# Kernel tuning notes

Measured on AMD Instinct MI355X. Metric: run time of the kernel, lower is better.

The kernel has to match this reference:

```python
import jax, jax.numpy as jnp
import numpy as np
from jax import lax

B, T, L = 32, 64, 1500        # flows, max packets per flow, packet length (MTU)
H, DC = 128, 100              # lstm hidden, cnn feature dim
KS, ST = 5, 3                 # conv kernel/stride
FLAT = 54 * 32                # conv output length 1500->499->165->54, 32 channels


def setup_inputs() -> dict:
    key = jax.random.key(0)
    ks = jax.random.split(key, 12)
    s = 0.05
    X = jax.random.normal(ks[0], (B, T, L), jnp.float32)
    lengths = jax.random.randint(ks[1], (B,), 1, T + 1, dtype=jnp.int32)
    conv1_w = jax.random.normal(ks[2], (128, 1, KS), jnp.float32) * s
    conv2_w = jax.random.normal(ks[3], (32, 128, KS), jnp.float32) * s
    conv3_w = jax.random.normal(ks[4], (32, 32, KS), jnp.float32) * s
    lin_w = jax.random.normal(ks[5], (DC, FLAT), jnp.float32) * s
    w_ih0 = jax.random.normal(ks[6], (4 * H, DC), jnp.float32) * s
    w_hh0 = jax.random.normal(ks[7], (4 * H, H), jnp.float32) * s
    w_ih1 = jax.random.normal(ks[8], (4 * H, H), jnp.float32) * s
    w_hh1 = jax.random.normal(ks[9], (4 * H, H), jnp.float32) * s
    fc1_w = jax.random.normal(ks[10], (10, H), jnp.float32) * s
    fc2_w = jax.random.normal(ks[11], (2, 10), jnp.float32) * s
    return {"X": X, "lengths": lengths, "conv1_w": conv1_w, "conv2_w": conv2_w,
            "conv3_w": conv3_w, "lin_w": lin_w, "w_ih0": w_ih0, "w_hh0": w_hh0,
            "w_ih1": w_ih1, "w_hh1": w_hh1, "fc1_w": fc1_w, "fc2_w": fc2_w}


def _conv(x, w):
    # x: [N, Cin, L], w: [Cout, Cin, K] -> valid conv, stride 3 (torch Conv1d semantics)
    return lax.conv_general_dilated(x, w, (ST,), 'VALID',
                                    dimension_numbers=('NCH', 'OIH', 'NCH'))


def _lstm_layer(xs, mask, w_ih, w_hh):
    # xs: [T, B, D]; mask: [T, B] (True = valid step); no biases (bias=False)
    Bn = xs.shape[1]
    h0 = jnp.zeros((Bn, H), xs.dtype)
    c0 = jnp.zeros((Bn, H), xs.dtype)

    def step(carry, inp):
        h, c = carry
        x_t, m_t = inp
        gates = x_t @ w_ih.T + h @ w_hh.T          # [B, 4H]
        i, f, g, o = jnp.split(gates, 4, axis=-1)  # torch gate order i,f,g,o
        i, f, o = jax.nn.sigmoid(i), jax.nn.sigmoid(f), jax.nn.sigmoid(o)
        g = jnp.tanh(g)
        c_new = f * c + i * g
        h_new = o * jnp.tanh(c_new)
        m = m_t[:, None]
        h = jnp.where(m, h_new, h)  # freeze state past each flow's length
        c = jnp.where(m, c_new, c)
        return (h, c), h

    (h_f, c_f), hs = lax.scan(step, (h0, c0), (xs, mask))
    return hs, h_f


def reference(X, lengths, conv1_w, conv2_w, conv3_w, lin_w,
              w_ih0, w_hh0, w_ih1, w_hh1, fc1_w, fc2_w):
    leaky = jax.nn.leaky_relu  # slope 0.01 matches torch default
    # ODCNN over every packet (batched over all B*T packets instead of python loops)
    x = X.reshape(B * T, 1, L)
    x = leaky(_conv(x, conv1_w))   # [BT, 128, 499]
    x = leaky(_conv(x, conv2_w))   # [BT, 32, 165]
    x = leaky(_conv(x, conv3_w))   # [BT, 32, 54]
    feats = x.reshape(B * T, FLAT) @ lin_w.T          # [BT, 100] (no activation)
    feats = feats.reshape(B, T, DC).transpose(1, 0, 2)  # [T, B, 100]
    mask = jnp.arange(T)[:, None] < lengths[None, :]     # [T, B]
    hs1, _ = _lstm_layer(feats, mask, w_ih0, w_hh0)
    _, h2 = _lstm_layer(hs1, mask, w_ih1, w_hh1)         # h at step len-1, top layer
    out = leaky(h2 @ fc1_w.T)
    out = leaky(out @ fc2_w.T)                           # [B, out_dim]
    return out
```

## Files before the change

### kernel.cpp

```cpp
#include <hip/hip_runtime.h>
#include <hip/hip_bf16.h>

#define B_ 32
#define T_ 64
#define H_ 128
#define L3OUT 54
#define FLAT_ 1728

typedef __attribute__((ext_vector_type(8))) short bf16x8;
typedef __attribute__((ext_vector_type(4))) float f32x4;

__device__ __forceinline__ float leakyf(float v) { return v > 0.f ? v : 0.01f * v; }
__device__ __forceinline__ float sigmoidf_(float v) { return 1.f / (1.f + expf(-v)); }
__device__ __forceinline__ unsigned int bf16rne(float v) {
  unsigned int b = __float_as_uint(v);
  return (b + 0x7FFFu + ((b >> 16) & 1u)) >> 16;
}
__device__ __forceinline__ unsigned int pk2bf(float lo, float hi) {
  __hip_bfloat162 h2 = __float22bfloat162_rn(make_float2(lo, hi));
  return *reinterpret_cast<unsigned int*>(&h2);
}
__device__ __forceinline__ bf16x8 ldb8(const unsigned short* p) {
  return *(const bf16x8*)p;
}
__device__ __forceinline__ void barrier_lgkm() {
  asm volatile("s_waitcnt lgkmcnt(0)\n\ts_barrier" ::: "memory");
}

__global__ __launch_bounds__(256) void k_prep(
    const float* __restrict__ w1, const float* __restrict__ w2,
    const float* __restrict__ w3, const float* __restrict__ linw,
    const float* __restrict__ wih0, const float* __restrict__ whh0,
    const float* __restrict__ wih1, const float* __restrict__ whh1,
    unsigned short* __restrict__ w1eh, unsigned short* __restrict__ w1el,
    unsigned short* __restrict__ w2h, unsigned short* __restrict__ w2l,
    unsigned short* __restrict__ w3h, unsigned short* __restrict__ w3l,
    unsigned short* __restrict__ linwh, unsigned short* __restrict__ linwl,
    unsigned short* __restrict__ wih0h, unsigned short* __restrict__ wih0l,
    float* __restrict__ whh0T, float* __restrict__ wih1T,
    float* __restrict__ whh1T) {
  const int e = blockIdx.x * 256 + threadIdx.x;
  if (e >= 264960) {
    int e5 = e - 264960;
    int m = e5 >> 16, r = e5 & 65535;
    int k = r >> 9, j = r & 511;
    const float* src = (m == 0) ? whh0 : ((m == 1) ? wih1 : whh1);
    float* dst = (m == 0) ? whh0T : ((m == 1) ? wih1T : whh1T);
    dst[r] = src[j * 128 + k];
    return;
  }
  float v;
  unsigned short* dh;
  unsigned short* dl;
  int di;
  if (e < 20480) {
    int cc = e / 5120, rem = e - cc * 5120;
    int c2 = rem / 160, r = rem - c2 * 160;
    int tap = r >> 5, c1l = r & 31;
    v = w2[c2 * 640 + (cc * 32 + c1l) * 5 + tap];
    dh = w2h; dl = w2l; di = e;
  } else if (e < 25600) {
    int e2 = e - 20480;
    int c3 = e2 / 160, r = e2 - c3 * 160;
    int tap = r >> 5, c2 = r & 31;
    v = w3[c3 * 160 + c2 * 5 + tap];
    dh = w3h; dl = w3l; di = e2;
  } else if (e < 198400) {
    int e3 = e - 25600;
    v = linw[e3];
    dh = linwh; dl = linwl; di = e3;
  } else if (e < 263936) {
    int e4 = e - 198400;
    int g = e4 >> 7, k = e4 & 127;
    v = (k < 100) ? wih0[g * 100 + k] : 0.f;
    dh = wih0h; dl = wih0l; di = e4;
  } else {
    int i = e - 263936;
    int c1 = i >> 3, j = i & 7;
    v = (j < 5) ? w1[c1 * 5 + j] : 0.f;
    dh = w1eh; dl = w1el; di = i;
  }
  unsigned int hb = bf16rne(v);
  float hf = __uint_as_float(hb << 16);
  unsigned int lb = bf16rne(v - hf);
  dh[di] = (unsigned short)hb;
  dl[di] = (unsigned short)lb;
}

__global__ __launch_bounds__(512) void k_conv123(
    const float* __restrict__ X, const float* __restrict__ w1,
    const unsigned short* __restrict__ w2h, const unsigned short* __restrict__ w2l,
    const unsigned short* __restrict__ w3h, const unsigned short* __restrict__ w3l,
    unsigned short* __restrict__ s3g) {
  __shared__ __align__(16) float Xs[1504];
  __shared__ __align__(16) unsigned int AhU[10640];

  const int n = blockIdx.x;
  const int tid = threadIdx.x;
  const int lane = tid & 63;
  const int w = tid >> 6;
  const int l15 = lane & 15;
  const int cg = lane >> 4;

  const float* Xn = X + (size_t)n * 1500;
  for (int i = tid; i < 1500; i += 512) Xs[i] = Xn[i];
  if (tid < 4) Xs[1500 + tid] = 0.f;
  for (int i = tid; i < 640; i += 512) AhU[10000 + i] = 0u;
  barrier_lgkm();

  float x0 = 0.f, x1 = 0.f, x2 = 0.f, x3 = 0.f, x4 = 0.f;
  if (tid < 500) {
    const float* xp = Xs + 3 * tid;
    x0 = xp[0]; x1 = xp[1]; x2 = xp[2]; x3 = xp[3]; x4 = xp[4];
  }

  f32x4 acc2[2][2];
#pragma unroll
  for (int a = 0; a < 2; ++a)
#pragma unroll
    for (int m = 0; m < 2; ++m) acc2[a][m] = (f32x4){0.f, 0.f, 0.f, 0.f};

  for (int cc = 0; cc < 4; ++cc) {
    barrier_lgkm();
    if (tid < 500) {
      const float* wc = w1 + cc * 160;
      unsigned int rowbuf[16];
#pragma unroll
      for (int p = 0; p < 16; ++p) {
        const float* wa = wc + 10 * p;
        float vA = fmaf(x4, wa[4], fmaf(x3, wa[3], fmaf(x2, wa[2], fmaf(x1, wa[1], x0 * wa[0]))));
        float vB = fmaf(x4, wa[9], fmaf(x3, wa[8], fmaf(x2, wa[7], fmaf(x1, wa[6], x0 * wa[5]))));
        vA = fmaxf(vA, 0.01f * vA);
        vB = fmaxf(vB, 0.01f * vB);
        rowbuf[p] = pk2bf(vA, vB);
      }
#pragma unroll
      for (int q = 0; q < 4; ++q)
        *(uint4*)(&AhU[tid * 20 + 4 * q]) = *(uint4*)(&rowbuf[4 * q]);
    }
    barrier_lgkm();
    const unsigned short* w2hB = w2h + cc * 5120;
    const unsigned short* w2lB = w2l + cc * 5120;
#pragma unroll
    for (int tap = 0; tap < 5; ++tap) {
      const int wc = tap * 32 + cg * 8;
      bf16x8 ah0 = ldb8(w2hB + l15 * 160 + wc);
      bf16x8 ah1 = ldb8(w2hB + (l15 + 16) * 160 + wc);
      bf16x8 al0 = ldb8(w2lB + l15 * 160 + wc);
      bf16x8 al1 = ldb8(w2lB + (l15 + 16) * 160 + wc);
      {
        bf16x8 bfr = ldb8((const unsigned short*)AhU + (3 * (w * 16 + l15) + tap) * 40 + cg * 8);
        acc2[0][0] = __builtin_amdgcn_mfma_f32_16x16x32_bf16(ah0, bfr, acc2[0][0], 0, 0, 0);
        acc2[0][0] = __builtin_amdgcn_mfma_f32_16x16x32_bf16(al0, bfr, acc2[0][0], 0, 0, 0);
        acc2[0][1] = __builtin_amdgcn_mfma_f32_16x16x32_bf16(ah1, bfr, acc2[0][1], 0, 0, 0);
        acc2[0][1] = __builtin_amdgcn_mfma_f32_16x16x32_bf16(al1, bfr, acc2[0][1], 0, 0, 0);
      }
      if (w < 3) {
        int nt = 8 + w;
        bf16x8 bfr = ldb8((const unsigned short*)AhU + (3 * (nt * 16 + l15) + tap) * 40 + cg * 8);
        acc2[1][0] = __builtin_amdgcn_mfma_f32_16x16x32_bf16(ah0, bfr, acc2[1][0], 0, 0, 0);
        acc2[1][0] = __builtin_amdgcn_mfma_f32_16x16x32_bf16(al0, bfr, acc2[1][0], 0, 0, 0);
        acc2[1][1] = __builtin_amdgcn_mfma_f32_16x16x32_bf16(ah1, bfr, acc2[1][1], 0, 0, 0);
        acc2[1][1] = __builtin_amdgcn_mfma_f32_16x16x32_bf16(al1, bfr, acc2[1][1], 0, 0, 0);
      }
    }
  }
  barrier_lgkm();
  for (int i = tid; i < 400; i += 512) AhU[176 * 20 + i] = 0u;
#pragma unroll
  for (int nti = 0; nti < 2; ++nti) {
    int nt = (nti == 0) ? w : (8 + w);
    if (nti == 0 || w < 3) {
      int l2 = nt * 16 + l15;
#pragma unroll
      for (int mt = 0; mt < 2; ++mt) {
#pragma unroll
        for (int j = 0; j < 2; ++j) {
          float e0 = leakyf(acc2[nti][mt][2 * j]);
          float e1 = leakyf(acc2[nti][mt][2 * j + 1]);
          AhU[l2 * 20 + mt * 8 + cg * 2 + j] = pk2bf(e0, e1);
        }
      }
    }
  }
  barrier_lgkm();
  if (w < 4) {
    f32x4 a3[2];
    a3[0] = (f32x4){0.f, 0.f, 0.f, 0.f};
    a3[1] = (f32x4){0.f, 0.f, 0.f, 0.f};
#pragma unroll
    for (int tap = 0; tap < 5; ++tap) {
      const int wc = tap * 32 + cg * 8;
      bf16x8 wh0 = ldb8(w3h + l15 * 160 + wc);
      bf16x8 wh1 = ldb8(w3h + (l15 + 16) * 160 + wc);
      bf16x8 wl0 = ldb8(w3l + l15 * 160 + wc);
      bf16x8 wl1 = ldb8(w3l + (l15 + 16) * 160 + wc);
      bf16x8 bfr = ldb8((const unsigned short*)AhU + (3 * (w * 16 + l15) + tap) * 40 + cg * 8);
      a3[0] = __builtin_amdgcn_mfma_f32_16x16x32_bf16(wh0, bfr, a3[0], 0, 0, 0);
      a3[0] = __builtin_amdgcn_mfma_f32_16x16x32_bf16(wl0, bfr, a3[0], 0, 0, 0);
      a3[1] = __builtin_amdgcn_mfma_f32_16x16x32_bf16(wh1, bfr, a3[1], 0, 0, 0);
      a3[1] = __builtin_amdgcn_mfma_f32_16x16x32_bf16(wl1, bfr, a3[1], 0, 0, 0);
    }
    int l3 = w * 16 + l15;
    if (l3 < L3OUT) {
#pragma unroll
      for (int mt = 0; mt < 2; ++mt) {
#pragma unroll
        for (int r = 0; r < 4; ++r) {
          int c3 = mt * 16 + cg * 4 + r;
          s3g[(size_t)n * FLAT_ + c3 * L3OUT + l3] = (unsigned short)bf16rne(leakyf(a3[mt][r]));
        }
      }
    }
  }
}

__global__ __launch_bounds__(448) void k_gemm_fx(
    const unsigned short* __restrict__ s3g,
    const unsigned short* __restrict__ linwh, const unsigned short* __restrict__ linwl,
    const unsigned short* __restrict__ wih0h, const unsigned short* __restrict__ wih0l,
    float* __restrict__ xg0) {
  __shared__ __align__(16) unsigned short fehS[16][136];
  __shared__ __align__(16) unsigned short felS[16][136];

  const int m0 = blockIdx.x * 16;
  const int tid = threadIdx.x;
  const int lane = tid & 63;
  const int w = tid >> 6;
  const int l15 = lane & 15;
  const int cg = lane >> 4;

  if (tid < 192) {
    int r = tid / 12, c = tid - r * 12;
    ((unsigned int*)&fehS[r][112])[c] = 0u;
    ((unsigned int*)&felS[r][112])[c] = 0u;
  }

  int brow = w * 16 + l15;
  if (brow > 99) brow = 99;
  const unsigned short* ap = s3g + (size_t)(m0 + l15) * FLAT_ + cg * 8;
  const unsigned short* bhp = linwh + (size_t)brow * FLAT_ + cg * 8;
  const unsigned short* blp = linwl + (size_t)brow * FLAT_ + cg * 8;

  f32x4 acc = (f32x4){0.f, 0.f, 0.f, 0.f};
#pragma unroll 6
  for (int ks = 0; ks < 54; ++ks) {
    bf16x8 af = ldb8(ap + ks * 32);
    bf16x8 bh = ldb8(bhp + ks * 32);
    bf16x8 bl = ldb8(blp + ks * 32);
    acc = __builtin_amdgcn_mfma_f32_16x16x32_bf16(af, bh, acc, 0, 0, 0);
    acc = __builtin_amdgcn_mfma_f32_16x16x32_bf16(af, bl, acc, 0, 0, 0);
  }
  const int jcol = w * 16 + l15;
#pragma unroll
  for (int r = 0; r < 4; ++r) {
    float v = acc[r];
    unsigned int hb = bf16rne(v);
    float hf = __uint_as_float(hb << 16);
    unsigned int lb = bf16rne(v - hf);
    fehS[cg * 4 + r][jcol] = (unsigned short)hb;
    felS[cg * 4 + r][jcol] = (unsigned short)lb;
  }
  __syncthreads();

#pragma unroll
  for (int nt0 = 0; nt0 < 5; ++nt0) {
    int nt = w + 7 * nt0;
    if (nt < 32) {
      f32x4 a = (f32x4){0.f, 0.f, 0.f, 0.f};
#pragma unroll
      for (int ks = 0; ks < 4; ++ks) {
        bf16x8 ah = ldb8(&fehS[l15][ks * 32 + cg * 8]);
        bf16x8 al = ldb8(&felS[l15][ks * 32 + cg * 8]);
        int br = nt * 16 + l15;
        bf16x8 bh = ldb8(wih0h + (size_t)br * 128 + ks * 32 + cg * 8);
        bf16x8 bl = ldb8(wih0l + (size_t)br * 128 + ks * 32 + cg * 8);
        a = __builtin_amdgcn_mfma_f32_16x16x32_bf16(ah, bh, a, 0, 0, 0);
        a = __builtin_amdgcn_mfma_f32_16x16x32_bf16(ah, bl, a, 0, 0, 0);
        a = __builtin_amdgcn_mfma_f32_16x16x32_bf16(al, bh, a, 0, 0, 0);
      }
#pragma unroll
      for (int r = 0; r < 4; ++r)
        xg0[(size_t)(m0 + cg * 4 + r) * 512 + nt * 16 + l15] = a[r];
    }
  }
}

__global__ __launch_bounds__(512) void k_lstm0(
    const float* __restrict__ xg0, const float* __restrict__ whh0T,
    const int* __restrict__ lengths, float* __restrict__ hs1) {
  __shared__ __align__(16) float h0s[H_];
  __shared__ float ps[16 * 128];
  __shared__ float gs[512];
  const int b = blockIdx.x;
  const int tid = threadIdx.x;
  const int ks = tid >> 7;
  const int jj = tid & 127;
  float w[4][32];
#pragma unroll
  for (int kk = 0; kk < 32; ++kk) {
#pragma unroll
    for (int q = 0; q < 4; ++q)
      w[q][kk] = whh0T[(ks * 32 + kk) * 512 + q * 128 + jj];
  }
  if (tid < H_) h0s[tid] = 0.f;
  float c = 0.f;
  const int len = lengths[b];
  float xcur = xg0[(size_t)(b * T_) * 512 + tid];
  barrier_lgkm();
  for (int t = 0; t < len; ++t) {
    float xnxt = (t + 1 < len) ? xg0[(size_t)(b * T_ + t + 1) * 512 + tid] : 0.f;
    float p0 = 0.f, p1 = 0.f, p2 = 0.f, p3 = 0.f;
#pragma unroll
    for (int k4 = 0; k4 < 8; ++k4) {
      float4 hv = *(const float4*)(h0s + ks * 32 + k4 * 4);
      p0 = fmaf(hv.x, w[0][k4 * 4], fmaf(hv.y, w[0][k4 * 4 + 1], fmaf(hv.z, w[0][k4 * 4 + 2], fmaf(hv.w, w[0][k4 * 4 + 3], p0))));
      p1 = fmaf(hv.x, w[1][k4 * 4], fmaf(hv.y, w[1][k4 * 4 + 1], fmaf(hv.z, w[1][k4 * 4 + 2], fmaf(hv.w, w[1][k4 * 4 + 3], p1))));
      p2 = fmaf(hv.x, w[2][k4 * 4], fmaf(hv.y, w[2][k4 * 4 + 1], fmaf(hv.z, w[2][k4 * 4 + 2], fmaf(hv.w, w[2][k4 * 4 + 3], p2))));
      p3 = fmaf(hv.x, w[3][k4 * 4], fmaf(hv.y, w[3][k4 * 4 + 1], fmaf(hv.z, w[3][k4 * 4 + 2], fmaf(hv.w, w[3][k4 * 4 + 3], p3))));
    }
    ps[(ks * 4 + 0) * 128 + jj] = p0;
    ps[(ks * 4 + 1) * 128 + jj] = p1;
    ps[(ks * 4 + 2) * 128 + jj] = p2;
    ps[(ks * 4 + 3) * 128 + jj] = p3;
    barrier_lgkm();
    {
      float gsum = xcur + ((ps[(0 * 4 + ks) * 128 + jj] + ps[(1 * 4 + ks) * 128 + jj]) +
                           (ps[(2 * 4 + ks) * 128 + jj] + ps[(3 * 4 + ks) * 128 + jj]));
      gs[tid] = (ks == 2) ? tanhf(gsum) : sigmoidf_(gsum);
    }
    barrier_lgkm();
    if (tid < H_) {
      float ig = gs[jj];
      float fg = gs[128 + jj];
      float gt = gs[256 + jj];
      float og = gs[384 + jj];
      c = fg * c + ig * gt;
      float hn = og * tanhf(c);
      h0s[jj] = hn;
      hs1[((size_t)(b * T_ + t)) * H_ + jj] = hn;
    }
    barrier_lgkm();
    xcur = xnxt;
  }
}

__global__ __launch_bounds__(512) void k_xg1(
    const float* __restrict__ hs1, const float* __restrict__ wih1T,
    float* __restrict__ xg1) {
  __shared__ __align__(16) float hsS[8][128];
  const int r0 = blockIdx.x * 8;
  const int tid = threadIdx.x;
  for (int i = tid; i < 8 * 128; i += 512) ((float*)hsS)[i] = hs1[(size_t)r0 * 128 + i];
  __syncthreads();
  float acc[8] = {0.f, 0.f, 0.f, 0.f, 0.f, 0.f, 0.f, 0.f};
#pragma unroll 4
  for (int k4 = 0; k4 < 32; ++k4) {
    float w0 = wih1T[(4 * k4 + 0) * 512 + tid];
    float w1v = wih1T[(4 * k4 + 1) * 512 + tid];
    float w2v = wih1T[(4 * k4 + 2) * 512 + tid];
    float w3v = wih1T[(4 * k4 + 3) * 512 + tid];
#pragma unroll
    for (int i = 0; i < 8; ++i) {
      float4 h = *(const float4*)(&hsS[i][4 * k4]);
      acc[i] += h.x * w0 + h.y * w1v + h.z * w2v + h.w * w3v;
    }
  }
#pragma unroll
  for (int i = 0; i < 8; ++i) xg1[((size_t)(r0 + i)) * 512 + tid] = acc[i];
}

__global__ __launch_bounds__(512) void k_lstm1(
    const float* __restrict__ xg1, const float* __restrict__ whh1T,
    const float* __restrict__ fc1, const float* __restrict__ fc2,
    const int* __restrict__ lengths, float* __restrict__ out) {
  __shared__ __align__(16) float h1s[H_];
  __shared__ float ps[16 * 128];
  __shared__ float gs[512];
  __shared__ float tmp10[10];
  const int b = blockIdx.x;
  const int tid = threadIdx.x;
  const int ks = tid >> 7;
  const int jj = tid & 127;
  float w[4][32];
#pragma unroll
  for (int kk = 0; kk < 32; ++kk) {
#pragma unroll
    for (int q = 0; q < 4; ++q)
      w[q][kk] = whh1T[(ks * 32 + kk) * 512 + q * 128 + jj];
  }
  if (tid < H_) h1s[tid] = 0.f;
  float c = 0.f;
  const int len = lengths[b];
  float xcur = xg1[(size_t)(b * T_) * 512 + tid];
  barrier_lgkm();
  for (int t = 0; t < len; ++t) {
    float xnxt = (t + 1 < len) ? xg1[(size_t)(b * T_ + t + 1) * 512 + tid] : 0.f;
    float p0 = 0.f, p1 = 0.f, p2 = 0.f, p3 = 0.f;
#pragma unroll
    for (int k4 = 0; k4 < 8; ++k4) {
      float4 hv = *(const float4*)(h1s + ks * 32 + k4 * 4);
      p0 = fmaf(hv.x, w[0][k4 * 4], fmaf(hv.y, w[0][k4 * 4 + 1], fmaf(hv.z, w[0][k4 * 4 + 2], fmaf(hv.w, w[0][k4 * 4 + 3], p0))));
      p1 = fmaf(hv.x, w[1][k4 * 4], fmaf(hv.y, w[1][k4 * 4 + 1], fmaf(hv.z, w[1][k4 * 4 + 2], fmaf(hv.w, w[1][k4 * 4 + 3], p1))));
      p2 = fmaf(hv.x, w[2][k4 * 4], fmaf(hv.y, w[2][k4 * 4 + 1], fmaf(hv.z, w[2][k4 * 4 + 2], fmaf(hv.w, w[2][k4 * 4 + 3], p2))));
      p3 = fmaf(hv.x, w[3][k4 * 4], fmaf(hv.y, w[3][k4 * 4 + 1], fmaf(hv.z, w[3][k4 * 4 + 2], fmaf(hv.w, w[3][k4 * 4 + 3], p3))));
    }
    ps[(ks * 4 + 0) * 128 + jj] = p0;
    ps[(ks * 4 + 1) * 128 + jj] = p1;
    ps[(ks * 4 + 2) * 128 + jj] = p2;
    ps[(ks * 4 + 3) * 128 + jj] = p3;
    barrier_lgkm();
    {
      float gsum = xcur + ((ps[(0 * 4 + ks) * 128 + jj] + ps[(1 * 4 + ks) * 128 + jj]) +
                           (ps[(2 * 4 + ks) * 128 + jj] + ps[(3 * 4 + ks) * 128 + jj]));
      gs[tid] = (ks == 2) ? tanhf(gsum) : sigmoidf_(gsum);
    }
    barrier_lgkm();
    if (tid < H_) {
      float ig = gs[jj];
      float fg = gs[128 + jj];
      float gt = gs[256 + jj];
      float og = gs[384 + jj];
      c = fg * c + ig * gt;
      float hn = og * tanhf(c);
      h1s[jj] = hn;
    }
    barrier_lgkm();
    xcur = xnxt;
  }
  if (tid < 10) {
    const float* fr = fc1 + tid * H_;
    float s = 0.f;
#pragma unroll 4
    for (int k = 0; k < H_; ++k) s += h1s[k] * fr[k];
    tmp10[tid] = leakyf(s);
  }
  barrier_lgkm();
  if (tid < 2) {
    const float* fr = fc2 + tid * 10;
    float s = 0.f;
#pragma unroll
    for (int j = 0; j < 10; ++j) s += tmp10[j] * fr[j];
    out[b * 2 + tid] = leakyf(s);
  }
}

extern "C" void kernel_launch(void* const* d_in, const int* in_sizes, int n_in,
                              void* d_out, int out_size, void* d_ws, size_t ws_size,
                              hipStream_t stream) {
  const float* X = (const float*)d_in[0];
  const int* lengths = (const int*)d_in[1];
  const float* w1 = (const float*)d_in[2];
  const float* w2 = (const float*)d_in[3];
  const float* w3 = (const float*)d_in[4];
  const float* linw = (const float*)d_in[5];
  const float* wih0 = (const float*)d_in[6];
  const float* whh0 = (const float*)d_in[7];
  const float* wih1 = (const float*)d_in[8];
  const float* whh1 = (const float*)d_in[9];
  const float* fc1 = (const float*)d_in[10];
  const float* fc2 = (const float*)d_in[11];

  char* wsb = (char*)d_ws;
  size_t off = 0;
  auto alloc = [&](size_t bytes) {
    char* p = wsb + off;
    off += (bytes + 511) & ~(size_t)511;
    return p;
  };
  unsigned short* s3g = (unsigned short*)alloc(2048 * 1728 * 2);
  float* xg0 = (float*)alloc(2048 * 512 * 4);
  unsigned short* w1eh = (unsigned short*)alloc(1024 * 2);
  unsigned short* w1el = (unsigned short*)alloc(1024 * 2);
  unsigned short* w2h = (unsigned short*)alloc(20480 * 2);
  unsigned short* w2l = (unsigned short*)alloc(20480 * 2);
  unsigned short* w3h = (unsigned short*)alloc(5120 * 2);
  unsigned short* w3l = (unsigned short*)alloc(5120 * 2);
  unsigned short* linwh = (unsigned short*)alloc(172800 * 2);
  unsigned short* linwl = (unsigned short*)alloc(172800 * 2);
  unsigned short* wih0h = (unsigned short*)alloc(65536 * 2);
  unsigned short* wih0l = (unsigned short*)alloc(65536 * 2);
  float* whh0T = (float*)alloc(65536 * 4);
  float* wih1T = (float*)alloc(65536 * 4);
  float* whh1T = (float*)alloc(65536 * 4);
  float* hs1 = (float*)alloc(262144 * 4);
  float* xg1 = (float*)alloc(2048 * 512 * 4);

  k_prep<<<1803, 256, 0, stream>>>(w1, w2, w3, linw, wih0, whh0, wih1, whh1,
                                   w1eh, w1el, w2h, w2l, w3h, w3l,
                                   linwh, linwl, wih0h, wih0l,
                                   whh0T, wih1T, whh1T);
  k_conv123<<<2048, 512, 0, stream>>>(X, w1, w2h, w2l, w3h, w3l, s3g);
  k_gemm_fx<<<128, 448, 0, stream>>>(s3g, linwh, linwl, wih0h, wih0l, xg0);
  k_lstm0<<<32, 512, 0, stream>>>(xg0, whh0T, lengths, hs1);
  k_xg1<<<256, 512, 0, stream>>>(hs1, wih1T, xg1);
  k_lstm1<<<32, 512, 0, stream>>>(xg1, whh1T, fc1, fc2, lengths, (float*)d_out);
}
```

Measured before the change: 268.2 us.

## Fuse both LSTM layers into one wavefront-pipelined kernel with flag handoff

Replaces the three serial kernels (layer-0 LSTM, input projection for layer 1, layer-1 LSTM) with one 64-block kernel. Blocks 0-31 run layer 0 and, after every 16 timesteps, compute that chunk's layer-1 input gates with split-bf16 MFMA and then publish a per-flow flag. Blocks 32-63 spin on those flags and run layer 1 concurrently, lagging one chunk behind. This removes two launches and the serial dependency between layers. In exchange it relies on all 64 blocks being co-resident, adds spin-wait and atomic overhead, and adds extra prep work and a memset.

Measured after the change: 255.3 us (median of 2 runs). 4.8% less time.

```diff
diff --git a/kernel.cpp b/kernel.cpp
--- a/kernel.cpp
+++ b/kernel.cpp
@@ -37,10 +37,11 @@
     unsigned short* __restrict__ w3h, unsigned short* __restrict__ w3l,
     unsigned short* __restrict__ linwh, unsigned short* __restrict__ linwl,
     unsigned short* __restrict__ wih0h, unsigned short* __restrict__ wih0l,
+    unsigned short* __restrict__ wih1h, unsigned short* __restrict__ wih1l,
     float* __restrict__ whh0T, float* __restrict__ wih1T,
     float* __restrict__ whh1T) {
   const int e = blockIdx.x * 256 + threadIdx.x;
-  if (e >= 264960) {
+  if (e >= 264960 && e < 461568) {
     int e5 = e - 264960;
     int m = e5 >> 16, r = e5 & 65535;
     int k = r >> 9, j = r & 511;
@@ -74,11 +75,15 @@
     int g = e4 >> 7, k = e4 & 127;
     v = (k < 100) ? wih0[g * 100 + k] : 0.f;
     dh = wih0h; dl = wih0l; di = e4;
-  } else {
+  } else if (e < 264960) {
     int i = e - 263936;
     int c1 = i >> 3, j = i & 7;
     v = (j < 5) ? w1[c1 * 5 + j] : 0.f;
     dh = w1eh; dl = w1el; di = i;
+  } else {
+    int e6 = e - 461568;
+    v = wih1[e6];
+    dh = wih1h; dl = wih1l; di = e6;
   }
   unsigned int hb = bf16rne(v);
   float hf = __uint_as_float(hb << 16);
@@ -286,162 +291,182 @@
   }
 }
 
-__global__ __launch_bounds__(512) void k_lstm0(
+__global__ __launch_bounds__(512) void k_lstm_fused(
     const float* __restrict__ xg0, const float* __restrict__ whh0T,
-    const int* __restrict__ lengths, float* __restrict__ hs1) {
-  __shared__ __align__(16) float h0s[H_];
+    const float* __restrict__ whh1T,
+    const unsigned short* __restrict__ wih1h, const unsigned short* __restrict__ wih1l,
+    const float* __restrict__ fc1, const float* __restrict__ fc2,
+    const int* __restrict__ lengths, float* __restrict__ xg1,
+    int* __restrict__ flags, float* __restrict__ out) {
+  __shared__ __align__(16) float hs[H_];
   __shared__ float ps[16 * 128];
   __shared__ float gs[512];
-  const int b = blockIdx.x;
+  __shared__ __align__(16) unsigned short hBh[16][136];
+  __shared__ __align__(16) unsigned short hBl[16][136];
+  __shared__ float tmp10[10];
+
+  const int bid = blockIdx.x;
   const int tid = threadIdx.x;
+  const int lane = tid & 63;
+  const int wv = tid >> 6;
+  const int l15 = lane & 15;
+  const int cg = lane >> 4;
   const int ks = tid >> 7;
   const int jj = tid & 127;
-  float w[4][32];
-#pragma unroll
-  for (int kk = 0; kk < 32; ++kk) {
-#pragma unroll
-    for (int q = 0; q < 4; ++q)
-      w[q][kk] = whh0T[(ks * 32 + kk) * 512 + q * 128 + jj];
-  }
-  if (tid < H_) h0s[tid] = 0.f;
-  float c = 0.f;
-  const int len = lengths[b];
-  float xcur = xg0[(size_t)(b * T_) * 512 + tid];
-  barrier_lgkm();
-  for (int t = 0; t < len; ++t) {
-    float xnxt = (t + 1 < len) ? xg0[(size_t)(b * T_ + t + 1) * 512 + tid] : 0.f;
-    float p0 = 0.f, p1 = 0.f, p2 = 0.f, p3 = 0.f;
-#pragma unroll
-    for (int k4 = 0; k4 < 8; ++k4) {
-      float4 hv = *(const float4*)(h0s + ks * 32 + k4 * 4);
-      p0 = fmaf(hv.x, w[0][k4 * 4], fmaf(hv.y, w[0][k4 * 4 + 1], fmaf(hv.z, w[0][k4 * 4 + 2], fmaf(hv.w, w[0][k4 * 4 + 3], p0))));
-      p1 = fmaf(hv.x, w[1][k4 * 4], fmaf(hv.y, w[1][k4 * 4 + 1], fmaf(hv.z, w[1][k4 * 4 + 2], fmaf(hv.w, w[1][k4 * 4 + 3], p1))));
-      p2 = fmaf(hv.x, w[2][k4 * 4], fmaf(hv.y, w[2][k4 * 4 + 1], fmaf(hv.z, w[2][k4 * 4 + 2], fmaf(hv.w, w[2][k4 * 4 + 3], p2))));
-      p3 = fmaf(hv.x, w[3][k4 * 4], fmaf(hv.y, w[3][k4 * 4 + 1], fmaf(hv.z, w[3][k4 * 4 + 2], fmaf(hv.w, w[3][k4 * 4 + 3], p3))));
-    }
-    ps[(ks * 4 + 0) * 128 + jj] = p0;
-    ps[(ks * 4 + 1) * 128 + jj] = p1;
-    ps[(ks * 4 + 2) * 128 + jj] = p2;
-    ps[(ks * 4 + 3) * 128 + jj] = p3;
+
+  if (bid < 32) {
+    const int b = bid;
+    float w[4][32];
+#pragma unroll
+    for (int kk = 0; kk < 32; ++kk) {
+#pragma unroll
+      for (int q = 0; q < 4; ++q)
+        w[q][kk] = whh0T[(ks * 32 + kk) * 512 + q * 128 + jj];
+    }
+    if (tid < H_) hs[tid] = 0.f;
+    float c = 0.f;
+    const int len = lengths[b];
+    float xcur = xg0[(size_t)(b * T_) * 512 + tid];
     barrier_lgkm();
-    {
-      float gsum = xcur + ((ps[(0 * 4 + ks) * 128 + jj] + ps[(1 * 4 + ks) * 128 + jj]) +
-                           (ps[(2 * 4 + ks) * 128 + jj] + ps[(3 * 4 + ks) * 128 + jj]));
-      gs[tid] = (ks == 2) ? tanhf(gsum) : sigmoidf_(gsum);
-    }
+    for (int ck = 0; ck < 4; ++ck) {
+      const int t0 = ck * 16;
+      if (t0 >= len) break;
+      for (int ts = 0; ts < 16; ++ts) {
+        const int t = t0 + ts;
+        if (t >= len) break;
+        float xnxt = (t + 1 < len) ? xg0[(size_t)(b * T_ + t + 1) * 512 + tid] : 0.f;
+        float p0 = 0.f, p1 = 0.f, p2 = 0.f, p3 = 0.f;
+#pragma unroll
+        for (int k4 = 0; k4 < 8; ++k4) {
+          float4 hv = *(const float4*)(hs + ks * 32 + k4 * 4);
+          p0 = fmaf(hv.x, w[0][k4 * 4], fmaf(hv.y, w[0][k4 * 4 + 1], fmaf(hv.z, w[0][k4 * 4 + 2], fmaf(hv.w, w[0][k4 * 4 + 3], p0))));
+          p1 = fmaf(hv.x, w[1][k4 * 4], fmaf(hv.y, w[1][k4 * 4 + 1], fmaf(hv.z, w[1][k4 * 4 + 2], fmaf(hv.w, w[1][k4 * 4 + 3], p1))));
+          p2 = fmaf(hv.x, w[2][k4 * 4], fmaf(hv.y, w[2][k4 * 4 + 1], fmaf(hv.z, w[2][k4 * 4 + 2], fmaf(hv.w, w[2][k4 * 4 + 3], p2))));
+          p3 = fmaf(hv.x, w[3][k4 * 4], fmaf(hv.y, w[3][k4 * 4 + 1], fmaf(hv.z, w[3][k4 * 4 + 2], fmaf(hv.w, w[3][k4 * 4 + 3], p3))));
+        }
+        ps[(ks * 4 + 0) * 128 + jj] = p0;
+        ps[(ks * 4 + 1) * 128 + jj] = p1;
+        ps[(ks * 4 + 2) * 128 + jj] = p2;
+        ps[(ks * 4 + 3) * 128 + jj] = p3;
+        barrier_lgkm();
+        {
+          float gsum = xcur + ((ps[(0 * 4 + ks) * 128 + jj] + ps[(1 * 4 + ks) * 128 + jj]) +
+                               (ps[(2 * 4 + ks) * 128 + jj] + ps[(3 * 4 + ks) * 128 + jj]));
+          gs[tid] = (ks == 2) ? tanhf(gsum) : sigmoidf_(gsum);
+        }
+        barrier_lgkm();
+        if (tid < H_) {
+          float ig = gs[jj];
+          float fg = gs[128 + jj];
+          float gt = gs[256 + jj];
+          float og = gs[384 + jj];
+          c = fg * c + ig * gt;
+          float hn = og * tanhf(c);
+          hs[jj] = hn;
+          unsigned int hb = bf16rne(hn);
+          hBh[ts][jj] = (unsigned short)hb;
+          float hf = __uint_as_float(hb << 16);
+          hBl[ts][jj] = (unsigned short)bf16rne(hn - hf);
+        }
+        barrier_lgkm();
+        xcur = xnxt;
+      }
+#pragma unroll
+      for (int mt4 = 0; mt4 < 4; ++mt4) {
+        const int mt = wv * 4 + mt4;
+        f32x4 a = (f32x4){0.f, 0.f, 0.f, 0.f};
+#pragma unroll
+        for (int kst = 0; kst < 4; ++kst) {
+          bf16x8 bh = ldb8(&hBh[l15][kst * 32 + cg * 8]);
+          bf16x8 bl = ldb8(&hBl[l15][kst * 32 + cg * 8]);
+          const int ar = mt * 16 + l15;
+          bf16x8 awh = ldb8(wih1h + (size_t)ar * 128 + kst * 32 + cg * 8);
+          bf16x8 awl = ldb8(wih1l + (size_t)ar * 128 + kst * 32 + cg * 8);
+          a = __builtin_amdgcn_mfma_f32_16x16x32_bf16(awh, bh, a, 0, 0, 0);
+          a = __builtin_amdgcn_mfma_f32_16x16x32_bf16(awl, bh, a, 0, 0, 0);
+          a = __builtin_amdgcn_mfma_f32_16x16x32_bf16(awh, bl, a, 0, 0, 0);
+        }
+        *(float4*)&xg1[(size_t)(b * T_ + t0 + l15) * 512 + mt * 16 + cg * 4] =
+            *(float4*)&a;
+      }
+      __syncthreads();
+      if (tid == 0)
+        __hip_atomic_store(flags + b, ck + 1, __ATOMIC_RELEASE, __HIP_MEMORY_SCOPE_AGENT);
+    }
+  } else {
+    const int b = bid - 32;
+    float w[4][32];
+#pragma unroll
+    for (int kk = 0; kk < 32; ++kk) {
+#pragma unroll
+      for (int q = 0; q < 4; ++q)
+        w[q][kk] = whh1T[(ks * 32 + kk) * 512 + q * 128 + jj];
+    }
+    if (tid < H_) hs[tid] = 0.f;
+    float c = 0.f;
+    const int len = lengths[b];
+    const float* xg1r = xg1 + (size_t)b * T_ * 512;
+    float xcur = 0.f;
     barrier_lgkm();
-    if (tid < H_) {
-      float ig = gs[jj];
-      float fg = gs[128 + jj];
-      float gt = gs[256 + jj];
-      float og = gs[384 + jj];
-      c = fg * c + ig * gt;
-      float hn = og * tanhf(c);
-      h0s[jj] = hn;
-      hs1[((size_t)(b * T_ + t)) * H_ + jj] = hn;
+    for (int t = 0; t < len; ++t) {
+      if ((t & 15) == 0) {
+        const int ck = t >> 4;
+        if (tid == 0) {
+          while (__hip_atomic_load(flags + b, __ATOMIC_ACQUIRE, __HIP_MEMORY_SCOPE_AGENT) <= ck)
+            __builtin_amdgcn_s_sleep(2);
+        }
+        __syncthreads();
+        xcur = xg1r[(size_t)t * 512 + tid];
+      }
+      float xnxt = ((((t + 1) & 15) != 0) && (t + 1 < len))
+                       ? xg1r[(size_t)(t + 1) * 512 + tid] : 0.f;
+      float p0 = 0.f, p1 = 0.f, p2 = 0.f, p3 = 0.f;
+#pragma unroll
+      for (int k4 = 0; k4 < 8; ++k4) {
+        float4 hv = *(const float4*)(hs + ks * 32 + k4 * 4);
+        p0 = fmaf(hv.x, w[0][k4 * 4], fmaf(hv.y, w[0][k4 * 4 + 1], fmaf(hv.z, w[0][k4 * 4 + 2], fmaf(hv.w, w[0][k4 * 4 + 3], p0))));
+        p1 = fmaf(hv.x, w[1][k4 * 4], fmaf(hv.y, w[1][k4 * 4 + 1], fmaf(hv.z, w[1][k4 * 4 + 2], fmaf(hv.w, w[1][k4 * 4 + 3], p1))));
+        p2 = fmaf(hv.x, w[2][k4 * 4], fmaf(hv.y, w[2][k4 * 4 + 1], fmaf(hv.z, w[2][k4 * 4 + 2], fmaf(hv.w, w[2][k4 * 4 + 3], p2))));
+        p3 = fmaf(hv.x, w[3][k4 * 4], fmaf(hv.y, w[3][k4 * 4 + 1], fmaf(hv.z, w[3][k4 * 4 + 2], fmaf(hv.w, w[3][k4 * 4 + 3], p3))));
+      }
+      ps[(ks * 4 + 0) * 128 + jj] = p0;
+      ps[(ks * 4 + 1) * 128 + jj] = p1;
+      ps[(ks * 4 + 2) * 128 + jj] = p2;
+      ps[(ks * 4 + 3) * 128 + jj] = p3;
+      barrier_lgkm();
+      {
+        float gsum = xcur + ((ps[(0 * 4 + ks) * 128 + jj] + ps[(1 * 4 + ks) * 128 + jj]) +
+                             (ps[(2 * 4 + ks) * 128 + jj] + ps[(3 * 4 + ks) * 128 + jj]));
+        gs[tid] = (ks == 2) ? tanhf(gsum) : sigmoidf_(gsum);
+      }
+      barrier_lgkm();
+      if (tid < H_) {
+        float ig = gs[jj];
+        float fg = gs[128 + jj];
+        float gt = gs[256 + jj];
+        float og = gs[384 + jj];
+        c = fg * c + ig * gt;
+        float hn = og * tanhf(c);
+        hs[jj] = hn;
+      }
+      barrier_lgkm();
+      xcur = xnxt;
+    }
+    if (tid < 10) {
+      const float* fr = fc1 + tid * H_;
+      float s = 0.f;
+#pragma unroll 4
+      for (int k = 0; k < H_; ++k) s += hs[k] * fr[k];
+      tmp10[tid] = leakyf(s);
     }
     barrier_lgkm();
-    xcur = xnxt;
-  }
-}
-
-__global__ __launch_bounds__(512) void k_xg1(
-    const float* __restrict__ hs1, const float* __restrict__ wih1T,
-    float* __restrict__ xg1) {
-  __shared__ __align__(16) float hsS[8][128];
-  const int r0 = blockIdx.x * 8;
-  const int tid = threadIdx.x;
-  for (int i = tid; i < 8 * 128; i += 512) ((float*)hsS)[i] = hs1[(size_t)r0 * 128 + i];
-  __syncthreads();
-  float acc[8] = {0.f, 0.f, 0.f, 0.f, 0.f, 0.f, 0.f, 0.f};
-#pragma unroll 4
-  for (int k4 = 0; k4 < 32; ++k4) {
-    float w0 = wih1T[(4 * k4 + 0) * 512 + tid];
-    float w1v = wih1T[(4 * k4 + 1) * 512 + tid];
-    float w2v = wih1T[(4 * k4 + 2) * 512 + tid];
-    float w3v = wih1T[(4 * k4 + 3) * 512 + tid];
-#pragma unroll
-    for (int i = 0; i < 8; ++i) {
-      float4 h = *(const float4*)(&hsS[i][4 * k4]);
-      acc[i] += h.x * w0 + h.y * w1v + h.z * w2v + h.w * w3v;
-    }
-  }
-#pragma unroll
-  for (int i = 0; i < 8; ++i) xg1[((size_t)(r0 + i)) * 512 + tid] = acc[i];
-}
-
-__global__ __launch_bounds__(512) void k_lstm1(
-    const float* __restrict__ xg1, const float* __restrict__ whh1T,
-    const float* __restrict__ fc1, const float* __restrict__ fc2,
-    const int* __restrict__ lengths, float* __restrict__ out) {
-  __shared__ __align__(16) float h1s[H_];
-  __shared__ float ps[16 * 128];
-  __shared__ float gs[512];
-  __shared__ float tmp10[10];
-  const int b = blockIdx.x;
-  const int tid = threadIdx.x;
-  const int ks = tid >> 7;
-  const int jj = tid & 127;
-  float w[4][32];
-#pragma unroll
-  for (int kk = 0; kk < 32; ++kk) {
-#pragma unroll
-    for (int q = 0; q < 4; ++q)
-      w[q][kk] = whh1T[(ks * 32 + kk) * 512 + q * 128 + jj];
-  }
-  if (tid < H_) h1s[tid] = 0.f;
-  float c = 0.f;
-  const int len = lengths[b];
-  float xcur = xg1[(size_t)(b * T_) * 512 + tid];
-  barrier_lgkm();
-  for (int t = 0; t < len; ++t) {
-    float xnxt = (t + 1 < len) ? xg1[(size_t)(b * T_ + t + 1) * 512 + tid] : 0.f;
-    float p0 = 0.f, p1 = 0.f, p2 = 0.f, p3 = 0.f;
-#pragma unroll
-    for (int k4 = 0; k4 < 8; ++k4) {
-      float4 hv = *(const float4*)(h1s + ks * 32 + k4 * 4);
-      p0 = fmaf(hv.x, w[0][k4 * 4], fmaf(hv.y, w[0][k4 * 4 + 1], fmaf(hv.z, w[0][k4 * 4 + 2], fmaf(hv.w, w[0][k4 * 4 + 3], p0))));
-      p1 = fmaf(hv.x, w[1][k4 * 4], fmaf(hv.y, w[1][k4 * 4 + 1], fmaf(hv.z, w[1][k4 * 4 + 2], fmaf(hv.w, w[1][k4 * 4 + 3], p1))));
-      p2 = fmaf(hv.x, w[2][k4 * 4], fmaf(hv.y, w[2][k4 * 4 + 1], fmaf(hv.z, w[2][k4 * 4 + 2], fmaf(hv.w, w[2][k4 * 4 + 3], p2))));
-      p3 = fmaf(hv.x, w[3][k4 * 4], fmaf(hv.y, w[3][k4 * 4 + 1], fmaf(hv.z, w[3][k4 * 4 + 2], fmaf(hv.w, w[3][k4 * 4 + 3], p3))));
-    }
-    ps[(ks * 4 + 0) * 128 + jj] = p0;
-    ps[(ks * 4 + 1) * 128 + jj] = p1;
-    ps[(ks * 4 + 2) * 128 + jj] = p2;
-    ps[(ks * 4 + 3) * 128 + jj] = p3;
-    barrier_lgkm();
-    {
-      float gsum = xcur + ((ps[(0 * 4 + ks) * 128 + jj] + ps[(1 * 4 + ks) * 128 + jj]) +
-                           (ps[(2 * 4 + ks) * 128 + jj] + ps[(3 * 4 + ks) * 128 + jj]));
-      gs[tid] = (ks == 2) ? tanhf(gsum) : sigmoidf_(gsum);
-    }
-    barrier_lgkm();
-    if (tid < H_) {
-      float ig = gs[jj];
-      float fg = gs[128 + jj];
-      float gt = gs[256 + jj];
-      float og = gs[384 + jj];
-      c = fg * c + ig * gt;
-      float hn = og * tanhf(c);
-      h1s[jj] = hn;
-    }
-    barrier_lgkm();
-    xcur = xnxt;
-  }
-  if (tid < 10) {
-    const float* fr = fc1 + tid * H_;
-    float s = 0.f;
-#pragma unroll 4
-    for (int k = 0; k < H_; ++k) s += h1s[k] * fr[k];
-    tmp10[tid] = leakyf(s);
-  }
-  barrier_lgkm();
-  if (tid < 2) {
-    const float* fr = fc2 + tid * 10;
-    float s = 0.f;
-#pragma unroll
-    for (int j = 0; j < 10; ++j) s += tmp10[j] * fr[j];
-    out[b * 2 + tid] = leakyf(s);
+    if (tid < 2) {
+      const float* fr = fc2 + tid * 10;
+      float s = 0.f;
+#pragma unroll
+      for (int j = 0; j < 10; ++j) s += tmp10[j] * fr[j];
+      out[b * 2 + tid] = leakyf(s);
+    }
   }
 }
 
@@ -470,6 +495,8 @@
   };
   unsigned short* s3g = (unsigned short*)alloc(2048 * 1728 * 2);
   float* xg0 = (float*)alloc(2048 * 512 * 4);
+  float* xg1 = (float*)alloc(2048 * 512 * 4);
+  int* flags = (int*)alloc(32 * 4);
   unsigned short* w1eh = (unsigned short*)alloc(1024 * 2);
   unsigned short* w1el = (unsigned short*)alloc(1024 * 2);
   unsigned short* w2h = (unsigned short*)alloc(20480 * 2);
@@ -480,19 +507,20 @@
   unsigned short* linwl = (unsigned short*)alloc(172800 * 2);
   unsigned short* wih0h = (unsigned short*)alloc(65536 * 2);
   unsigned short* wih0l = (unsigned short*)alloc(65536 * 2);
+  unsigned short* wih1h = (unsigned short*)alloc(65536 * 2);
+  unsigned short* wih1l = (unsigned short*)alloc(65536 * 2);
   float* whh0T = (float*)alloc(65536 * 4);
   float* wih1T = (float*)alloc(65536 * 4);
   float* whh1T = (float*)alloc(65536 * 4);
-  float* hs1 = (float*)alloc(262144 * 4);
-  float* xg1 = (float*)alloc(2048 * 512 * 4);
-
-  k_prep<<<1803, 256, 0, stream>>>(w1, w2, w3, linw, wih0, whh0, wih1, whh1,
+
+  hipMemsetAsync(flags, 0, 32 * sizeof(int), stream);
+  k_prep<<<2059, 256, 0, stream>>>(w1, w2, w3, linw, wih0, whh0, wih1, whh1,
                                    w1eh, w1el, w2h, w2l, w3h, w3l,
-                                   linwh, linwl, wih0h, wih0l,
+                                   linwh, linwl, wih0h, wih0l, wih1h, wih1l,
                                    whh0T, wih1T, whh1T);
   k_conv123<<<2048, 512, 0, stream>>>(X, w1, w2h, w2l, w3h, w3l, s3g);
   k_gemm_fx<<<128, 448, 0, stream>>>(s3g, linwh, linwl, wih0h, wih0l, xg0);
-  k_lstm0<<<32, 512, 0, stream>>>(xg0, whh0T, lengths, hs1);
-  k_xg1<<<256, 512, 0, stream>>>(hs1, wih1T, xg1);
-  k_lstm1<<<32, 512, 0, stream>>>(xg1, whh1T, fc1, fc2, lengths, (float*)d_out);
-}
+  k_lstm_fused<<<64, 512, 0, stream>>>(xg0, whh0T, whh1T, wih1h, wih1l,
+                                       fc1, fc2, lengths, xg1, flags,
+                                       (float*)d_out);
+}
```
